# Kernel optimization log

Measured on AMD Instinct MI355X. Metric: run time of the kernel, lower is better.

The kernel has to match this reference:

```python
import jax, jax.numpy as jnp
import numpy as np

B, S, H = 4, 2048, 1024
NH, HD = 16, 64
LN_EPS = 1e-5


def _l2norm(x, axis=-1, eps=1e-12):
    n = jnp.sqrt(jnp.sum(x * x, axis=axis, keepdims=True))
    return x / jnp.maximum(n, eps)


def setup_inputs() -> dict:
    key = jax.random.key(0)
    ks = jax.random.split(key, 10)
    sd = 0.02
    x = jax.random.normal(ks[0], (B, S, H), jnp.float32)
    Wq = jax.random.normal(ks[1], (H, H), jnp.float32) * sd
    Wk = jax.random.normal(ks[2], (H, H), jnp.float32) * sd
    Wv = jax.random.normal(ks[3], (H, H), jnp.float32) * sd
    Wa = jax.random.normal(ks[4], (NH, H), jnp.float32) * sd
    ba = jnp.zeros((NH,), jnp.float32)
    Wb = jax.random.normal(ks[5], (NH, H), jnp.float32) * sd
    bb = jnp.zeros((NH,), jnp.float32)
    Wg = jax.random.normal(ks[6], (H, H), jnp.float32) * sd
    Wo = jax.random.normal(ks[7], (H, H), jnp.float32) * sd
    ln_g = jnp.ones((H,), jnp.float32)
    ln_b = jnp.zeros((H,), jnp.float32)
    return {"x": x, "Wq": Wq, "Wk": Wk, "Wv": Wv, "Wa": Wa, "ba": ba,
            "Wb": Wb, "bb": bb, "Wg": Wg, "Wo": Wo, "ln_g": ln_g, "ln_b": ln_b}


def _forward(x, Wq, Wk, Wv, Wa, ba, Wb, bb, Wg, Wo, ln_g, ln_b):
    q = _l2norm((x @ Wq.T).reshape(B, S, NH, HD))  # [B,S,nh,hd]
    k = _l2norm((x @ Wk.T).reshape(B, S, NH, HD))
    v = jax.nn.silu(x @ Wv.T).reshape(B, S, NH, HD)
    alpha = jax.nn.sigmoid(x @ Wa.T + ba)  # [B,S,nh]
    beta = jax.nn.sigmoid(x @ Wb.T + bb)   # [B,S,nh]

    def step(state, inp):
        a_t, b_t, k_t, v_t, q_t = inp  # a,b: [B,nh]; k,v,q: [B,nh,hd]
        a_ = a_t[:, :, None, None]
        b_ = b_t[:, :, None, None]
        kk = k_t[..., :, None] * k_t[..., None, :]  # [B,nh,hd,hd]
        state = a_ * state * (1.0 - b_ * kk) + b_ * (v_t[..., :, None] * k_t[..., None, :])
        out_t = jnp.sum(state * q_t[..., None, :], axis=-1)  # [B,nh,hd]
        return state, out_t

    # time-major xs for scan
    xs = (jnp.moveaxis(alpha, 1, 0), jnp.moveaxis(beta, 1, 0),
          jnp.moveaxis(k, 1, 0), jnp.moveaxis(v, 1, 0), jnp.moveaxis(q, 1, 0))
    state0 = jnp.zeros((B, NH, HD, HD), x.dtype)
    _, outs = jax.lax.scan(step, state0, xs)  # [S,B,nh,hd]
    out = jnp.moveaxis(outs, 0, 1).reshape(B, S, H)

    # LayerNorm over total_dim
    mu = jnp.mean(out, axis=-1, keepdims=True)
    var = jnp.var(out, axis=-1, keepdims=True)
    out = (out - mu) / jnp.sqrt(var + LN_EPS) * ln_g + ln_b

    out = out * jax.nn.silu(x @ Wg.T)
    return out @ Wo.T


def reference(x, Wq, Wk, Wv, Wa, ba, Wb, bb, Wg, Wo, ln_g, ln_b):
    return _forward(x, Wq, Wk, Wv, Wa, ba, Wb, bb, Wg, Wo, ln_g, ln_b)
```

## Files before the change

kernel.cpp:

```cpp
#include <hip/hip_runtime.h>

typedef unsigned short u16;
typedef __bf16 bf16x8 __attribute__((ext_vector_type(8)));
typedef float f32x4 __attribute__((ext_vector_type(4)));

constexpr int Bq  = 4;
constexpr int Sq  = 2048;
constexpr int Hq  = 1024;
constexpr int NHq = 16;
constexpr int HDq = 64;
constexpr int CCH = 16;
constexpr int LCH = 128;

constexpr size_t OFF_WB = 0;
constexpr size_t OFF_XB = 10485760;
constexpr size_t OFF_Q  = 27262976;
constexpr size_t OFF_K  = 60817408;
constexpr size_t OFF_V  = 94371840;
constexpr size_t OFF_G  = 127926272;
constexpr size_t OFF_AL = 161480704;
constexpr size_t OFF_BE = 162004992;
constexpr size_t OFF_P  = 162529280;
constexpr size_t OFF_O  = 179306496;

__device__ __forceinline__ u16 f2bf(float f) {
  unsigned u = __float_as_uint(f);
  u += 0x7fffu + ((u >> 16) & 1u);
  return (u16)(u >> 16);
}
__device__ __forceinline__ float sigmoidf_(float x) { return 1.f / (1.f + __expf(-x)); }

__device__ __forceinline__ void async16(const void* g, void* l) {
  __builtin_amdgcn_global_load_lds((const __attribute__((address_space(1))) void*)g,
                                   (__attribute__((address_space(3))) void*)l, 16, 0, 0);
}

__global__ __launch_bounds__(256) void cvt_x_kernel(const float* __restrict__ in, u16* __restrict__ outp) {
  const size_t i = ((size_t)blockIdx.x * 256 + threadIdx.x) * 4;
  float4 f = *(const float4*)(in + i);
  ushort4 u; u.x = f2bf(f.x); u.y = f2bf(f.y); u.z = f2bf(f.z); u.w = f2bf(f.w);
  *(ushort4*)(outp + i) = u;
}

__global__ __launch_bounds__(256) void cvt_w_kernel(const float* __restrict__ w0, const float* __restrict__ w1,
    const float* __restrict__ w2, const float* __restrict__ w3, const float* __restrict__ w4,
    u16* __restrict__ outp) {
  const int z = blockIdx.z;
  const float* src = (z == 0) ? w0 : (z == 1) ? w1 : (z == 2) ? w2 : (z == 3) ? w3 : w4;
  const size_t i = ((size_t)blockIdx.x * 256 + threadIdx.x) * 4;
  float4 f = *(const float4*)(src + i);
  ushort4 u; u.x = f2bf(f.x); u.y = f2bf(f.y); u.z = f2bf(f.z); u.w = f2bf(f.w);
  *(ushort4*)(outp + (size_t)z * (1024 * 1024) + i) = u;
}

__global__ __launch_bounds__(256) void cvt_ab_kernel(const float* __restrict__ Wa, const float* __restrict__ Wb,
    u16* __restrict__ outp) {
  const size_t i = ((size_t)blockIdx.x * 256 + threadIdx.x) * 4;
  const int row = (int)(i >> 10);
  ushort4 u;
  if (row < 32) {
    const float* src = (row < 16) ? (Wa + i) : (Wb + i - 16 * 1024);
    float4 f = *(const float4*)src;
    u.x = f2bf(f.x); u.y = f2bf(f.y); u.z = f2bf(f.z); u.w = f2bf(f.w);
  } else {
    u.x = u.y = u.z = u.w = 0;
  }
  *(ushort4*)(outp + i) = u;
}


__device__ __forceinline__ void lda4(bf16x8 af[4][2], const u16* LA, int wr, int mh, int l15, int qd, int l7) {
#pragma unroll
  for (int i = 0; i < 4; ++i)
#pragma unroll
    for (int kk = 0; kk < 2; ++kk)
      af[i][kk] = *(const bf16x8*)(LA + (wr * 128 + mh * 64 + i * 16 + l15) * 64 + (((kk * 4 + qd) ^ l7) * 8));
}
__device__ __forceinline__ void ldb2(bf16x8 bf[2][2], const u16* LB, int wc, int nh, int l15, int qd, int l7) {
#pragma unroll
  for (int j = 0; j < 2; ++j)
#pragma unroll
    for (int kk = 0; kk < 2; ++kk)
      bf[j][kk] = *(const bf16x8*)(LB + (wc * 64 + nh * 32 + j * 16 + l15) * 64 + (((kk * 4 + qd) ^ l7) * 8));
}
__device__ __forceinline__ void mm16(f32x4 acc[8][4], const bf16x8 af[4][2], const bf16x8 bf[2][2], int mh, int nh) {
#pragma unroll
  for (int i = 0; i < 4; ++i)
#pragma unroll
    for (int j = 0; j < 2; ++j) {
      f32x4 c = acc[mh * 4 + i][nh * 2 + j];
      c = __builtin_amdgcn_mfma_f32_16x16x32_bf16(af[i][0], bf[j][0], c, 0, 0, 0);
      c = __builtin_amdgcn_mfma_f32_16x16x32_bf16(af[i][1], bf[j][1], c, 0, 0, 0);
      acc[mh * 4 + i][nh * 2 + j] = c;
    }
}
__device__ __forceinline__ void stageH(u16* LD, int bufp, int mat, int h, const u16* gRow0, int kElem,
                                       int rr, int sl8, int wv) {
  const u16* s0 = gRow0 + (size_t)(h * 128 + rr) * 1024 + kElem + sl8;
  u16* d = LD + bufp * 32768 + mat * 16384 + h * 8192 + wv * 512;
  async16(s0, d);
  async16(s0 + (size_t)(64 * 1024), d + 4096);
}

template<int S1, int S2, int VM>
__device__ __forceinline__ void tile16(u16* LD, int bp, int kt,
    const u16* gA, const u16* gB, f32x4 acc[8][4], bf16x8 af[4][2], bf16x8 bf0[2][2], bf16x8 bf1[2][2],
    int wr, int wc, int l15, int qd, int l7, int rr, int sl8, int wv) {
  const u16* LA = LD + bp * 32768;
  const u16* LB = LA + 16384;
  lda4(af, LA, wr, 0, l15, qd, l7);
  ldb2(bf0, LB, wc, 0, l15, qd, l7);
  if (S1) stageH(LD, bp ^ 1, 0, 0, gA, (kt + 1) * 64, rr, sl8, wv);
  __builtin_amdgcn_s_barrier();
  asm volatile("s_waitcnt lgkmcnt(0)" ::: "memory");
  __builtin_amdgcn_sched_barrier(0);
  __builtin_amdgcn_s_setprio(1);
  mm16(acc, af, bf0, 0, 0);
  __builtin_amdgcn_s_setprio(0);
  __builtin_amdgcn_s_barrier();
  ldb2(bf1, LB, wc, 1, l15, qd, l7);
  if (S1) stageH(LD, bp ^ 1, 0, 1, gA, (kt + 1) * 64, rr, sl8, wv);
  __builtin_amdgcn_s_barrier();
  asm volatile("s_waitcnt lgkmcnt(0)" ::: "memory");
  __builtin_amdgcn_sched_barrier(0);
  __builtin_amdgcn_s_setprio(1);
  mm16(acc, af, bf1, 0, 1);
  __builtin_amdgcn_s_setprio(0);
  __builtin_amdgcn_s_barrier();
  lda4(af, LA, wr, 1, l15, qd, l7);
  if (S2) stageH(LD, bp, 1, 0, gB, (kt + 2) * 64, rr, sl8, wv);
  __builtin_amdgcn_s_barrier();
  asm volatile("s_waitcnt lgkmcnt(0)" ::: "memory");
  __builtin_amdgcn_sched_barrier(0);
  __builtin_amdgcn_s_setprio(1);
  mm16(acc, af, bf0, 1, 0);
  __builtin_amdgcn_s_setprio(0);
  __builtin_amdgcn_s_barrier();
  if (S2) stageH(LD, bp, 1, 1, gB, (kt + 2) * 64, rr, sl8, wv);
  __builtin_amdgcn_s_barrier();
  __builtin_amdgcn_sched_barrier(0);
  __builtin_amdgcn_s_setprio(1);
  mm16(acc, af, bf1, 1, 1);
  __builtin_amdgcn_s_setprio(0);
  if (VM == 4) asm volatile("s_waitcnt vmcnt(4)" ::: "memory");
  else if (VM == 0) asm volatile("s_waitcnt vmcnt(0)" ::: "memory");
  __builtin_amdgcn_s_barrier();
}

__global__ __launch_bounds__(512, 2) void gemm256(const u16* __restrict__ A, const u16* __restrict__ Wall,
    const u16* __restrict__ Wab,
    float* __restrict__ Cq, float* __restrict__ Ck, float* __restrict__ Cv, float* __restrict__ Cg,
    float* __restrict__ al, float* __restrict__ be,
    const float* __restrict__ ba, const float* __restrict__ bb, int mode) {
  __shared__ __align__(16) u16 Lds[65536];
  u16* LD = &Lds[0];
  const int tid = threadIdx.x;
  const int wv = tid >> 6, lane = tid & 63;
  const int l15 = lane & 15, qd = lane >> 4, l7 = l15 & 7;
  const int wr = wv >> 2, wc = wv & 3;
  const int rr = tid >> 3, sl8 = ((tid & 7) ^ (rr & 7)) * 8;

  int mx, ny, z;
  const u16* Wm;
  if (mode == 0) { mx = blockIdx.x & 31; ny = blockIdx.x >> 5; z = 0; Wm = Wall; }
  else if (blockIdx.x < 32) { mx = blockIdx.x; ny = 0; z = 4; Wm = Wab; }
  else {
    const int b = blockIdx.x - 32;
    mx = b & 31; ny = (b >> 5) & 3; z = b >> 7;
    Wm = Wall + (size_t)z * (1024 * 1024);
  }
  const int m0 = mx * 256, n0 = ny * 256;
  const u16* gA = A + (size_t)m0 * 1024;
  const u16* gB = Wm + (size_t)n0 * 1024;

  f32x4 acc[8][4] = {};
  bf16x8 af[4][2], bf0[2][2], bf1[2][2];

  stageH(LD, 0, 0, 0, gA, 0,  rr, sl8, wv);
  stageH(LD, 0, 0, 1, gA, 0,  rr, sl8, wv);
  stageH(LD, 0, 1, 0, gB, 0,  rr, sl8, wv);
  stageH(LD, 0, 1, 1, gB, 0,  rr, sl8, wv);
  stageH(LD, 1, 1, 0, gB, 64, rr, sl8, wv);
  stageH(LD, 1, 1, 1, gB, 64, rr, sl8, wv);
  asm volatile("s_waitcnt vmcnt(4)" ::: "memory");
  __builtin_amdgcn_s_barrier();

#pragma unroll 1
  for (int t2 = 0; t2 < 7; ++t2) {
    tile16<1, 1, 4>(LD, 0, 2 * t2,     gA, gB, acc, af, bf0, bf1, wr, wc, l15, qd, l7, rr, sl8, wv);
    tile16<1, 1, 4>(LD, 1, 2 * t2 + 1, gA, gB, acc, af, bf0, bf1, wr, wc, l15, qd, l7, rr, sl8, wv);
  }
  tile16<1, 0, 0>(LD, 0, 14, gA, gB, acc, af, bf0, bf1, wr, wc, l15, qd, l7, rr, sl8, wv);
  tile16<0, 0, -1>(LD, 1, 15, gA, gB, acc, af, bf0, bf1, wr, wc, l15, qd, l7, rr, sl8, wv);

  if (mode == 1 && z == 4) {
    if (wc == 0) {
      const float bav = ba[l15], bbv = bb[l15];
#pragma unroll
      for (int mi = 0; mi < 8; ++mi) {
        const int row = m0 + wr * 128 + mi * 16 + qd * 4;
#pragma unroll
        for (int r = 0; r < 4; ++r) {
          al[(size_t)(row + r) * 16 + l15] = sigmoidf_(acc[mi][0][r] + bav);
          be[(size_t)(row + r) * 16 + l15] = sigmoidf_(acc[mi][1][r] + bbv);
        }
      }
    }
    return;
  }
  if (mode == 1 && z <= 1) {
#pragma unroll
    for (int mi = 0; mi < 8; ++mi)
#pragma unroll
      for (int r = 0; r < 4; ++r) {
        float ss = acc[mi][0][r] * acc[mi][0][r] + acc[mi][1][r] * acc[mi][1][r]
                 + acc[mi][2][r] * acc[mi][2][r] + acc[mi][3][r] * acc[mi][3][r];
        ss += __shfl_xor(ss, 1); ss += __shfl_xor(ss, 2);
        ss += __shfl_xor(ss, 4); ss += __shfl_xor(ss, 8);
        const float rn = 1.f / fmaxf(sqrtf(ss), 1e-12f);
        acc[mi][0][r] *= rn; acc[mi][1][r] *= rn; acc[mi][2][r] *= rn; acc[mi][3][r] *= rn;
      }
  } else if (mode == 1 && z == 2) {
#pragma unroll
    for (int mi = 0; mi < 8; ++mi)
#pragma unroll
      for (int ni = 0; ni < 4; ++ni)
#pragma unroll
        for (int r = 0; r < 4; ++r)
          acc[mi][ni][r] = acc[mi][ni][r] * sigmoidf_(acc[mi][ni][r]);
  }
  float* C = (mode == 0) ? Cq : ((z == 0) ? Cq : (z == 1) ? Ck : (z == 2) ? Cv : Cg);
#pragma unroll
  for (int mi = 0; mi < 8; ++mi) {
    const int row = m0 + wr * 128 + mi * 16 + qd * 4;
#pragma unroll
    for (int ni = 0; ni < 4; ++ni) {
      const int col = n0 + wc * 64 + ni * 16 + l15;
#pragma unroll
      for (int r = 0; r < 4; ++r)
        C[(size_t)(row + r) * 1024 + col] = acc[mi][ni][r];
    }
  }
}

struct ScanLds1 { float kb[2][16 * 64]; float vb[2][16 * 64]; float ab[2][32]; };
struct ScanLds2 { float kb[2][16 * 64]; float qb[2][16 * 64]; float vb[2][16 * 64]; float ab[2][32]; };

__global__ __launch_bounds__(256, 4) void scan_p1(const float* __restrict__ k, const float* __restrict__ v,
    const float* __restrict__ al, const float* __restrict__ be,
    float* __restrict__ P, float* __restrict__ Q) {
  __shared__ ScanLds1 L;
  const int tid = threadIdx.x, wv = tid >> 6, lane = tid & 63;
  const int bh = blockIdx.x >> 4, c = blockIdx.x & 15;
  const int b = bh >> 4, h = bh & 15;
  const int rg = lane >> 3, cg = lane & 7;
  const int r0 = wv * 16 + rg * 2, c8 = cg * 8;
  const size_t base0 = ((size_t)(b * Sq + c * LCH)) * 1024 + h * 64;
  const size_t ab0   = ((size_t)(b * Sq + c * LCH)) * 16 + h;
  const int tokw = lane >> 4, seg = lane & 15;
  auto stage = [&](int tile, int bi) {
    #pragma unroll
    for (int j = 0; j < 2; ++j) {
      const int job = wv * 2 + j;
      const int arr = job >> 2, i = job & 3;
      const float* src = arr ? v : k;
      float* dst = arr ? &L.vb[bi][i * 256] : &L.kb[bi][i * 256];
      async16(src + base0 + (size_t)(tile * 16 + i * 4 + tokw) * 1024 + seg * 4, dst);
    }
    if (wv == 0 && lane < 32) {
      const int w16 = lane >> 4, tt = lane & 15;
      const float* s = w16 ? be : al;
      L.ab[bi][w16 * 16 + tt] = s[ab0 + (size_t)(tile * 16 + tt) * 16];
    }
  };
  float Pr[16], Qr[16];
  #pragma unroll
  for (int i = 0; i < 16; ++i) { Pr[i] = 1.f; Qr[i] = 0.f; }
  stage(0, 0);
  for (int tile = 0; tile < 8; ++tile) {
    __syncthreads();
    if (tile < 7) stage(tile + 1, (tile + 1) & 1);
    const int bi = tile & 1;
    const float* kbp = L.kb[bi];
    const float* vbp = L.vb[bi];
    const float* abp = L.ab[bi];
    #pragma unroll 2
    for (int tt = 0; tt < 16; ++tt) {
      const float a = abp[tt], bt = abp[16 + tt];
      float4 kcv0 = *(const float4*)(kbp + tt * 64 + c8);
      float4 kcv1 = *(const float4*)(kbp + tt * 64 + c8 + 4);
      float2 krvv = *(const float2*)(kbp + tt * 64 + r0);
      float2 vrvv = *(const float2*)(vbp + tt * 64 + r0);
      const float kcv[8] = {kcv0.x, kcv0.y, kcv0.z, kcv0.w, kcv1.x, kcv1.y, kcv1.z, kcv1.w};
      const float krv[2] = {krvv.x, krvv.y};
      const float vrv[2] = {vrvv.x, vrvv.y};
      const float abt = a * bt;
      float c1[2], c2[2];
      #pragma unroll
      for (int i = 0; i < 2; ++i) { c1[i] = abt * krv[i]; c2[i] = bt * vrv[i]; }
      #pragma unroll
      for (int i = 0; i < 2; ++i)
        #pragma unroll
        for (int j = 0; j < 8; ++j) {
          const int e = i * 8 + j;
          const float A = fmaf(-c1[i], kcv[j], a);
          Qr[e] = fmaf(A, Qr[e], c2[i] * kcv[j]);
          Pr[e] *= A;
        }
    }
  }
  const size_t pbase = ((size_t)bh * CCH + c) * 4096 + (size_t)c8;
  #pragma unroll
  for (int i = 0; i < 2; ++i) {
    const size_t pi = pbase + (size_t)(r0 + i) * 64;
    *(float4*)(P + pi)     = make_float4(Pr[i*8],   Pr[i*8+1], Pr[i*8+2], Pr[i*8+3]);
    *(float4*)(P + pi + 4) = make_float4(Pr[i*8+4], Pr[i*8+5], Pr[i*8+6], Pr[i*8+7]);
    *(float4*)(Q + pi)     = make_float4(Qr[i*8],   Qr[i*8+1], Qr[i*8+2], Qr[i*8+3]);
    *(float4*)(Q + pi + 4) = make_float4(Qr[i*8+4], Qr[i*8+5], Qr[i*8+6], Qr[i*8+7]);
  }
}

__global__ __launch_bounds__(256) void scan_comb(float* __restrict__ P, const float* __restrict__ Q) {
  const int g = blockIdx.x * 256 + threadIdx.x;
  const int elem = g & 4095;
  const int bh = g >> 12;
  float s = 0.f;
  for (int c = 0; c < CCH; ++c) {
    const size_t idx = ((size_t)bh * CCH + c) * 4096 + elem;
    const float p = P[idx], qq = Q[idx];
    P[idx] = s;
    s = fmaf(p, s, qq);
  }
}

__global__ __launch_bounds__(256, 4) void scan_p2(const float* __restrict__ q, const float* __restrict__ k,
    const float* __restrict__ v, const float* __restrict__ al, const float* __restrict__ be,
    const float* __restrict__ Pini, float* __restrict__ o) {
  __shared__ ScanLds2 L;
  const int tid = threadIdx.x, wv = tid >> 6, lane = tid & 63;
  const int bh = blockIdx.x >> 4, c = blockIdx.x & 15;
  const int b = bh >> 4, h = bh & 15;
  const int rg = lane >> 3, cg = lane & 7;
  const int r0 = wv * 16 + rg * 2, c8 = cg * 8;
  const size_t base0 = ((size_t)(b * Sq + c * LCH)) * 1024 + h * 64;
  const size_t ab0   = ((size_t)(b * Sq + c * LCH)) * 16 + h;
  const size_t pbase = ((size_t)bh * CCH + c) * 4096 + (size_t)c8;
  const int tokw = lane >> 4, seg = lane & 15;
  auto stage = [&](int tile, int bi) {
    #pragma unroll
    for (int j = 0; j < 3; ++j) {
      const int job = wv * 3 + j;
      const int arr = job >> 2, i = job & 3;
      const float* src = (arr == 0) ? k : (arr == 1) ? q : v;
      float* dst = (arr == 0) ? &L.kb[bi][i * 256] : (arr == 1) ? &L.qb[bi][i * 256]
                                                                : &L.vb[bi][i * 256];
      async16(src + base0 + (size_t)(tile * 16 + i * 4 + tokw) * 1024 + seg * 4, dst);
    }
    if (wv == 0 && lane < 32) {
      const int w16 = lane >> 4, tt = lane & 15;
      const float* s = w16 ? be : al;
      L.ab[bi][w16 * 16 + tt] = s[ab0 + (size_t)(tile * 16 + tt) * 16];
    }
  };
  float st[16];
  #pragma unroll
  for (int i = 0; i < 2; ++i) {
    float4 s0 = *(const float4*)(Pini + pbase + (size_t)(r0 + i) * 64);
    float4 s1 = *(const float4*)(Pini + pbase + (size_t)(r0 + i) * 64 + 4);
    st[i*8]   = s0.x; st[i*8+1] = s0.y; st[i*8+2] = s0.z; st[i*8+3] = s0.w;
    st[i*8+4] = s1.x; st[i*8+5] = s1.y; st[i*8+6] = s1.z; st[i*8+7] = s1.w;
  }
  stage(0, 0);
  const bool hi4 = (cg & 4);
  const int rowIdx = r0 + (cg >> 2);
  const bool doStore = ((cg & 3) == 0);
  for (int tile = 0; tile < 8; ++tile) {
    __syncthreads();
    if (tile < 7) stage(tile + 1, (tile + 1) & 1);
    const int bi = tile & 1;
    const float* kbp = L.kb[bi];
    const float* qbp = L.qb[bi];
    const float* vbp = L.vb[bi];
    const float* abp = L.ab[bi];
    #pragma unroll 2
    for (int tt = 0; tt < 16; ++tt) {
      const int t = tile * 16 + tt;
      const float a = abp[tt], bt = abp[16 + tt];
      float4 kcv0 = *(const float4*)(kbp + tt * 64 + c8);
      float4 kcv1 = *(const float4*)(kbp + tt * 64 + c8 + 4);
      float4 qcv0 = *(const float4*)(qbp + tt * 64 + c8);
      float4 qcv1 = *(const float4*)(qbp + tt * 64 + c8 + 4);
      float2 krvv = *(const float2*)(kbp + tt * 64 + r0);
      float2 vrvv = *(const float2*)(vbp + tt * 64 + r0);
      const float kcv[8] = {kcv0.x, kcv0.y, kcv0.z, kcv0.w, kcv1.x, kcv1.y, kcv1.z, kcv1.w};
      const float qcv[8] = {qcv0.x, qcv0.y, qcv0.z, qcv0.w, qcv1.x, qcv1.y, qcv1.z, qcv1.w};
      const float krv[2] = {krvv.x, krvv.y};
      const float vrv[2] = {vrvv.x, vrvv.y};
      const float abt = a * bt;
      float c1[2], c2[2];
      #pragma unroll
      for (int i = 0; i < 2; ++i) { c1[i] = abt * krv[i]; c2[i] = bt * vrv[i]; }
      float p[2];
      p[0] = 0.f; p[1] = 0.f;
      #pragma unroll
      for (int i = 0; i < 2; ++i)
        #pragma unroll
        for (int j = 0; j < 8; ++j) {
          const int e = i * 8 + j;
          const float A = fmaf(-c1[i], kcv[j], a);
          st[e] = fmaf(A, st[e], c2[i] * kcv[j]);
          p[i] = fmaf(st[e], qcv[j], p[i]);
        }
      float my    = hi4 ? p[1] : p[0];
      float other = hi4 ? p[0] : p[1];
      my += __shfl_xor(other, 4);
      my += __shfl_xor(my, 2);
      my += __shfl_xor(my, 1);
      if (doStore) o[base0 + (size_t)t * 1024 + rowIdx] = my;
    }
  }
}

__global__ __launch_bounds__(256) void ln_gate_kernel(const float* __restrict__ o, const float* __restrict__ g,
    const float* __restrict__ ln_g, const float* __restrict__ ln_b, u16* __restrict__ y) {
  const int t = blockIdx.x, tid = threadIdx.x;
  const size_t row = (size_t)t * 1024;
  float4 xv = *(const float4*)(o + row + tid * 4);
  float s  = xv.x + xv.y + xv.z + xv.w;
  float s2 = xv.x * xv.x + xv.y * xv.y + xv.z * xv.z + xv.w * xv.w;
  #pragma unroll
  for (int m = 1; m < 64; m <<= 1) { s += __shfl_xor(s, m); s2 += __shfl_xor(s2, m); }
  __shared__ float red[8];
  const int w = tid >> 6, lane = tid & 63;
  if (lane == 0) { red[w] = s; red[4 + w] = s2; }
  __syncthreads();
  s  = red[0] + red[1] + red[2] + red[3];
  s2 = red[4] + red[5] + red[6] + red[7];
  const float mu = s * (1.f / 1024.f);
  const float var = s2 * (1.f / 1024.f) - mu * mu;
  const float rstd = rsqrtf(var + 1e-5f);
  float4 gv = *(const float4*)(g + row + tid * 4);
  float4 lg = *(const float4*)(ln_g + tid * 4);
  float4 lb = *(const float4*)(ln_b + tid * 4);
  ushort4 u;
  u.x = f2bf(((xv.x - mu) * rstd * lg.x + lb.x) * (gv.x * sigmoidf_(gv.x)));
  u.y = f2bf(((xv.y - mu) * rstd * lg.y + lb.y) * (gv.y * sigmoidf_(gv.y)));
  u.z = f2bf(((xv.z - mu) * rstd * lg.z + lb.z) * (gv.z * sigmoidf_(gv.z)));
  u.w = f2bf(((xv.w - mu) * rstd * lg.w + lb.w) * (gv.w * sigmoidf_(gv.w)));
  *(ushort4*)(y + row + tid * 4) = u;
}

extern "C" void kernel_launch(void* const* d_in, const int* in_sizes, int n_in,
                              void* d_out, int out_size, void* d_ws, size_t ws_size,
                              hipStream_t stream) {
  const float* x    = (const float*)d_in[0];
  const float* Wq   = (const float*)d_in[1];
  const float* Wk   = (const float*)d_in[2];
  const float* Wv   = (const float*)d_in[3];
  const float* Wa   = (const float*)d_in[4];
  const float* ba   = (const float*)d_in[5];
  const float* Wb   = (const float*)d_in[6];
  const float* bb   = (const float*)d_in[7];
  const float* Wg   = (const float*)d_in[8];
  const float* Wo   = (const float*)d_in[9];
  const float* ln_g = (const float*)d_in[10];
  const float* ln_b = (const float*)d_in[11];
  float* out = (float*)d_out;
  char* ws = (char*)d_ws;

  u16*   wb  = (u16*)(ws + OFF_WB);
  u16*   xb  = (u16*)(ws + OFF_XB);
  float* qf  = (float*)(ws + OFF_Q);
  float* kf  = (float*)(ws + OFF_K);
  float* vf  = (float*)(ws + OFF_V);
  float* gf  = (float*)(ws + OFF_G);
  float* al  = (float*)(ws + OFF_AL);
  float* be  = (float*)(ws + OFF_BE);
  u16*   wab = (u16*)(ws + OFF_P);
  float* Pb  = (float*)(ws + OFF_P);
  float* Qc  = (float*)(ws + OFF_XB);
  float* of  = (float*)(ws + OFF_O);
  u16*   yb  = xb;

  cvt_x_kernel<<<8192, 256, 0, stream>>>(x, xb);
  cvt_w_kernel<<<dim3(1024, 1, 5), 256, 0, stream>>>(Wq, Wk, Wv, Wg, Wo, wb);
  cvt_ab_kernel<<<256, 256, 0, stream>>>(Wa, Wb, wab);
  gemm256<<<544, 512, 0, stream>>>(xb, wb, wab, qf, kf, vf, gf, al, be, ba, bb, 1);
  scan_p1<<<1024, 256, 0, stream>>>(kf, vf, al, be, Pb, Qc);
  scan_comb<<<1024, 256, 0, stream>>>(Pb, Qc);
  scan_p2<<<1024, 256, 0, stream>>>(qf, kf, vf, al, be, Pb, of);
  ln_gate_kernel<<<8192, 256, 0, stream>>>(of, gf, ln_g, ln_b, yb);
  gemm256<<<128, 512, 0, stream>>>(yb, wb + (size_t)4 * 1024 * 1024, wab,
                                   out, out, out, out, al, be, ba, bb, 0);
}
```

Measured before the change: 409.6 us.

## Split alpha/beta projection into dedicated small GEMM and remap GEMM block order

The 32-row alpha/beta projection, which used to pad a full 256-wide GEMM tile and waste most of its MFMA work, moves into its own lightweight ab_gemm kernel that loads operands straight from global memory. The main projection GEMM now launches 512 blocks instead of 544, and both GEMM launches remap blockIdx so that consecutive blocks spread across row and column tiles, which should improve L2 reuse and cache locality. The scan_p1 inner loop is unrolled further and the scan_comb loop is fully unrolled. The trade-off is an extra kernel launch, plus the new kernel's direct global loads, which get no LDS reuse.

After: 419.2 us. 2.3% more time.

```diff
diff --git a/kernel.cpp b/kernel.cpp
--- a/kernel.cpp
+++ b/kernel.cpp
@@ -57,17 +57,42 @@
     u16* __restrict__ outp) {
   const size_t i = ((size_t)blockIdx.x * 256 + threadIdx.x) * 4;
   const int row = (int)(i >> 10);
-  ushort4 u;
-  if (row < 32) {
-    const float* src = (row < 16) ? (Wa + i) : (Wb + i - 16 * 1024);
-    float4 f = *(const float4*)src;
-    u.x = f2bf(f.x); u.y = f2bf(f.y); u.z = f2bf(f.z); u.w = f2bf(f.w);
-  } else {
-    u.x = u.y = u.z = u.w = 0;
-  }
+  const float* src = (row < 16) ? (Wa + i) : (Wb + i - 16 * 1024);
+  float4 f = *(const float4*)src;
+  ushort4 u; u.x = f2bf(f.x); u.y = f2bf(f.y); u.z = f2bf(f.z); u.w = f2bf(f.w);
   *(ushort4*)(outp + i) = u;
 }
 
+__global__ __launch_bounds__(256) void ab_gemm(const u16* __restrict__ A, const u16* __restrict__ Wab,
+    float* __restrict__ al, float* __restrict__ be, const float* __restrict__ ba, const float* __restrict__ bb) {
+  const int tid = threadIdx.x, wv = tid >> 6, lane = tid & 63;
+  const int l15 = lane & 15, qd = lane >> 4;
+  const int m0 = blockIdx.x * 128 + wv * 32;
+  const u16* gA = A + (size_t)m0 * 1024 + qd * 8;
+  const u16* gB = Wab + (size_t)l15 * 1024 + qd * 8;
+  f32x4 acc[2][2] = {};
+#pragma unroll 4
+  for (int kt = 0; kt < 1024; kt += 32) {
+    bf16x8 a0 = *(const bf16x8*)(gA + (size_t)l15 * 1024 + kt);
+    bf16x8 a1 = *(const bf16x8*)(gA + (size_t)(16 + l15) * 1024 + kt);
+    bf16x8 b0 = *(const bf16x8*)(gB + kt);
+    bf16x8 b1 = *(const bf16x8*)(gB + 16 * 1024 + kt);
+    acc[0][0] = __builtin_amdgcn_mfma_f32_16x16x32_bf16(a0, b0, acc[0][0], 0, 0, 0);
+    acc[0][1] = __builtin_amdgcn_mfma_f32_16x16x32_bf16(a0, b1, acc[0][1], 0, 0, 0);
+    acc[1][0] = __builtin_amdgcn_mfma_f32_16x16x32_bf16(a1, b0, acc[1][0], 0, 0, 0);
+    acc[1][1] = __builtin_amdgcn_mfma_f32_16x16x32_bf16(a1, b1, acc[1][1], 0, 0, 0);
+  }
+  const float bav = ba[l15], bbv = bb[l15];
+#pragma unroll
+  for (int mi = 0; mi < 2; ++mi) {
+    const int row = m0 + mi * 16 + qd * 4;
+#pragma unroll
+    for (int r = 0; r < 4; ++r) {
+      al[(size_t)(row + r) * 16 + l15] = sigmoidf_(acc[mi][0][r] + bav);
+      be[(size_t)(row + r) * 16 + l15] = sigmoidf_(acc[mi][1][r] + bbv);
+    }
+  }
+}
 
 __device__ __forceinline__ void lda4(bf16x8 af[4][2], const u16* LA, int wr, int mh, int l15, int qd, int l7) {
 #pragma unroll
@@ -148,10 +173,8 @@
 }
 
 __global__ __launch_bounds__(512, 2) void gemm256(const u16* __restrict__ A, const u16* __restrict__ Wall,
-    const u16* __restrict__ Wab,
     float* __restrict__ Cq, float* __restrict__ Ck, float* __restrict__ Cv, float* __restrict__ Cg,
-    float* __restrict__ al, float* __restrict__ be,
-    const float* __restrict__ ba, const float* __restrict__ bb, int mode) {
+    int mode) {
   __shared__ __align__(16) u16 Lds[65536];
   u16* LD = &Lds[0];
   const int tid = threadIdx.x;
@@ -162,11 +185,12 @@
 
   int mx, ny, z;
   const u16* Wm;
-  if (mode == 0) { mx = blockIdx.x & 31; ny = blockIdx.x >> 5; z = 0; Wm = Wall; }
-  else if (blockIdx.x < 32) { mx = blockIdx.x; ny = 0; z = 4; Wm = Wab; }
-  else {
-    const int b = blockIdx.x - 32;
-    mx = b & 31; ny = (b >> 5) & 3; z = b >> 7;
+  if (mode == 0) {
+    const int job = ((blockIdx.x & 7) << 4) + (blockIdx.x >> 3);
+    mx = job & 31; ny = job >> 5; z = 0; Wm = Wall;
+  } else {
+    const int job = ((blockIdx.x & 7) << 6) + (blockIdx.x >> 3);
+    mx = job & 31; ny = (job >> 5) & 3; z = job >> 7;
     Wm = Wall + (size_t)z * (1024 * 1024);
   }
   const int m0 = mx * 256, n0 = ny * 256;
@@ -193,21 +217,6 @@
   tile16<1, 0, 0>(LD, 0, 14, gA, gB, acc, af, bf0, bf1, wr, wc, l15, qd, l7, rr, sl8, wv);
   tile16<0, 0, -1>(LD, 1, 15, gA, gB, acc, af, bf0, bf1, wr, wc, l15, qd, l7, rr, sl8, wv);
 
-  if (mode == 1 && z == 4) {
-    if (wc == 0) {
-      const float bav = ba[l15], bbv = bb[l15];
-#pragma unroll
-      for (int mi = 0; mi < 8; ++mi) {
-        const int row = m0 + wr * 128 + mi * 16 + qd * 4;
-#pragma unroll
-        for (int r = 0; r < 4; ++r) {
-          al[(size_t)(row + r) * 16 + l15] = sigmoidf_(acc[mi][0][r] + bav);
-          be[(size_t)(row + r) * 16 + l15] = sigmoidf_(acc[mi][1][r] + bbv);
-        }
-      }
-    }
-    return;
-  }
   if (mode == 1 && z <= 1) {
 #pragma unroll
     for (int mi = 0; mi < 8; ++mi)
@@ -284,7 +293,7 @@
     const float* kbp = L.kb[bi];
     const float* vbp = L.vb[bi];
     const float* abp = L.ab[bi];
-    #pragma unroll 2
+    #pragma unroll 4
     for (int tt = 0; tt < 16; ++tt) {
       const float a = abp[tt], bt = abp[16 + tt];
       float4 kcv0 = *(const float4*)(kbp + tt * 64 + c8);
@@ -325,6 +334,7 @@
   const int elem = g & 4095;
   const int bh = g >> 12;
   float s = 0.f;
+  #pragma unroll
   for (int c = 0; c < CCH; ++c) {
     const size_t idx = ((size_t)bh * CCH + c) * 4096 + elem;
     const float p = P[idx], qq = Q[idx];
@@ -386,14 +396,14 @@
     for (int tt = 0; tt < 16; ++tt) {
       const int t = tile * 16 + tt;
       const float a = abp[tt], bt = abp[16 + tt];
-      float4 kcv0 = *(const float4*)(kbp + tt * 64 + c8);
-      float4 kcv1 = *(const float4*)(kbp + tt * 64 + c8 + 4);
-      float4 qcv0 = *(const float4*)(qbp + tt * 64 + c8);
-      float4 qcv1 = *(const float4*)(qbp + tt * 64 + c8 + 4);
+      float4 kc0 = *(const float4*)(kbp + tt * 64 + c8);
+      float4 kc1 = *(const float4*)(kbp + tt * 64 + c8 + 4);
+      float4 qc0 = *(const float4*)(qbp + tt * 64 + c8);
+      float4 qc1 = *(const float4*)(qbp + tt * 64 + c8 + 4);
       float2 krvv = *(const float2*)(kbp + tt * 64 + r0);
       float2 vrvv = *(const float2*)(vbp + tt * 64 + r0);
-      const float kcv[8] = {kcv0.x, kcv0.y, kcv0.z, kcv0.w, kcv1.x, kcv1.y, kcv1.z, kcv1.w};
-      const float qcv[8] = {qcv0.x, qcv0.y, qcv0.z, qcv0.w, qcv1.x, qcv1.y, qcv1.z, qcv1.w};
+      const float kcv[8] = {kc0.x, kc0.y, kc0.z, kc0.w, kc1.x, kc1.y, kc1.z, kc1.w};
+      const float qcv[8] = {qc0.x, qc0.y, qc0.z, qc0.w, qc1.x, qc1.y, qc1.z, qc1.w};
       const float krv[2] = {krvv.x, krvv.y};
       const float vrv[2] = {vrvv.x, vrvv.y};
       const float abt = a * bt;
@@ -484,12 +494,12 @@
 
   cvt_x_kernel<<<8192, 256, 0, stream>>>(x, xb);
   cvt_w_kernel<<<dim3(1024, 1, 5), 256, 0, stream>>>(Wq, Wk, Wv, Wg, Wo, wb);
-  cvt_ab_kernel<<<256, 256, 0, stream>>>(Wa, Wb, wab);
-  gemm256<<<544, 512, 0, stream>>>(xb, wb, wab, qf, kf, vf, gf, al, be, ba, bb, 1);
+  cvt_ab_kernel<<<32, 256, 0, stream>>>(Wa, Wb, wab);
+  ab_gemm<<<64, 256, 0, stream>>>(xb, wab, al, be, ba, bb);
+  gemm256<<<512, 512, 0, stream>>>(xb, wb, qf, kf, vf, gf, 1);
   scan_p1<<<1024, 256, 0, stream>>>(kf, vf, al, be, Pb, Qc);
   scan_comb<<<1024, 256, 0, stream>>>(Pb, Qc);
   scan_p2<<<1024, 256, 0, stream>>>(qf, kf, vf, al, be, Pb, of);
   ln_gate_kernel<<<8192, 256, 0, stream>>>(of, gf, ln_g, ln_b, yb);
-  gemm256<<<128, 512, 0, stream>>>(yb, wb + (size_t)4 * 1024 * 1024, wab,
-                                   out, out, out, out, al, be, ba, bb, 0);
-}
+  gemm256<<<128, 512, 0, stream>>>(yb, wb + (size_t)4 * 1024 * 1024, out, out, out, out, 0);
+}
```
